# Kernel optimization log

Hardware: AMD Instinct MI355X
Metric: run time of the kernel (lower is better)

The kernel has to match this reference:

```python
import jax, jax.numpy as jnp
import numpy as np

D_MODEL = 2048
N_HEADS = 16
N_KV_HEADS = 4
HEAD_DIM = D_MODEL // N_HEADS  # 128
WINDOW = 512
THETA = 10000.0


def rotate_half(x):
    x1, x2 = jnp.split(x, 2, axis=-1)
    return jnp.concatenate((-x2, x1), axis=-1)


def rope_cos_sin(seq_len, dtype=jnp.float32):
    inv_freq = 1.0 / (THETA ** (jnp.arange(0, HEAD_DIM, 2, dtype=jnp.float32) / HEAD_DIM))
    t = jnp.arange(seq_len, dtype=jnp.float32)
    freqs = jnp.outer(t, inv_freq)              # [S, HEAD_DIM/2]
    emb = jnp.concatenate((freqs, freqs), -1)   # [S, HEAD_DIM]
    return jnp.cos(emb).astype(dtype), jnp.sin(emb).astype(dtype)


def setup_inputs() -> dict:
    key = jax.random.key(0)
    ks = jax.random.split(key, 5)
    B, S = 2, 2048
    sc = 1.0 / np.sqrt(D_MODEL)
    return {
        "x": jax.random.normal(ks[0], (B, S, D_MODEL), jnp.float32),
        "wq": jax.random.normal(ks[1], (D_MODEL, N_HEADS * HEAD_DIM), jnp.float32) * sc,
        "wk": jax.random.normal(ks[2], (D_MODEL, N_KV_HEADS * HEAD_DIM), jnp.float32) * sc,
        "wv": jax.random.normal(ks[3], (D_MODEL, N_KV_HEADS * HEAD_DIM), jnp.float32) * sc,
        "wo": jax.random.normal(ks[4], (N_HEADS * HEAD_DIM, D_MODEL), jnp.float32) * sc,
    }


def reference(x, wq, wk, wv, wo):
    B, S, _ = x.shape
    n_rep = N_HEADS // N_KV_HEADS

    q = (x @ wq).reshape(B, S, N_HEADS, HEAD_DIM).transpose(0, 2, 1, 3)      # [B,H,S,D]
    k = (x @ wk).reshape(B, S, N_KV_HEADS, HEAD_DIM).transpose(0, 2, 1, 3)   # [B,KVH,S,D]
    v = (x @ wv).reshape(B, S, N_KV_HEADS, HEAD_DIM).transpose(0, 2, 1, 3)

    cos, sin = rope_cos_sin(S, x.dtype)  # [S, D]
    q = q * cos + rotate_half(q) * sin
    k = k * cos + rotate_half(k) * sin

    # GQA: repeat kv heads to match query heads
    k = jnp.repeat(k, n_rep, axis=1)  # [B,H,S,D]
    v = jnp.repeat(v, n_rep, axis=1)

    scale = 1.0 / np.sqrt(HEAD_DIM)
    scores = jnp.einsum("bhqd,bhkd->bhqk", q, k) * scale

    # causal + sliding-window mask: allow i-WINDOW+1 <= j <= i
    i = jnp.arange(S)[:, None]
    j = jnp.arange(S)[None, :]
    allowed = (j <= i) & (j >= i - WINDOW + 1)
    scores = jnp.where(allowed, scores, -jnp.inf)

    attn = jax.nn.softmax(scores.astype(jnp.float32), axis=-1).astype(x.dtype)
    out = jnp.einsum("bhqk,bhkd->bhqd", attn, v)          # [B,H,S,D]
    out = out.transpose(0, 2, 1, 3).reshape(B, S, N_HEADS * HEAD_DIM)
    return out @ wo
```

## Files before the change

kernel.cpp:

```cpp
#include <hip/hip_runtime.h>
#include <math.h>


typedef unsigned short u16;
typedef __attribute__((ext_vector_type(4))) float f32x4;
typedef __attribute__((ext_vector_type(8))) __bf16 bf16x8;
typedef __attribute__((ext_vector_type(4))) __bf16 bf16x4;
typedef __attribute__((ext_vector_type(4))) short s16x4;
typedef __attribute__((ext_vector_type(8))) unsigned short u16x8;
typedef __attribute__((ext_vector_type(4))) unsigned short u16x4;

#define DEV static __device__ __forceinline__
#define WAITV(n) asm volatile("s_waitcnt vmcnt(" #n ")" ::: "memory")

DEV float bf2f(u16 h) {
    union { unsigned int i; float f; } x;
    x.i = ((unsigned int)h) << 16;
    return x.f;
}
DEV u16 f2bf(float f) {
    union { float f; unsigned int i; } x;
    x.f = f;
    unsigned int u = x.i;
    return (u16)((u + 0x7FFFu + ((u >> 16) & 1u)) >> 16);
}

DEV f32x4 mfma32(bf16x8 a, bf16x8 b, f32x4 c) {
    return __builtin_amdgcn_mfma_f32_16x16x32_bf16(a, b, c, 0, 0, 0);
}
DEV f32x4 mfma16(bf16x4 a, bf16x4 b, f32x4 c) {
#if __has_builtin(__builtin_amdgcn_mfma_f32_16x16x16_bf16)
    return __builtin_amdgcn_mfma_f32_16x16x16_bf16(a, b, c, 0, 0, 0);
#else
    union { bf16x4 v; s16x4 s; } ua, ub;
    ua.v = a; ub.v = b;
    return __builtin_amdgcn_mfma_f32_16x16x16bf16_1k(ua.s, ub.s, c, 0, 0, 0);
#endif
}

DEV void gload_lds16(const void* g, void* lds) {
    __builtin_amdgcn_global_load_lds(
        (const __attribute__((address_space(1))) unsigned int*)g,
        (__attribute__((address_space(3))) unsigned int*)lds, 16, 0, 0);
}

__global__ __launch_bounds__(256) void sincos_kernel(float* ct, float* st) {
    int idx = blockIdx.x * 256 + threadIdx.x;
    int s = idx >> 6, d = idx & 63;
    float inv = exp2f(-(float)d * (13.287712379549449f / 64.f));
    float a = (float)s * inv;
    float sv, cv;
    sincosf(a, &sv, &cv);
    ct[idx] = cv;
    st[idx] = sv;
}

__global__ __launch_bounds__(256) void f32_to_bf16_kernel(const float* in, u16* out, int n4) {
    int i = blockIdx.x * 256 + threadIdx.x;
    if (i >= n4) return;
    float4 v = ((const float4*)in)[i];
    u16x4 o;
    o[0] = f2bf(v.x); o[1] = f2bf(v.y); o[2] = f2bf(v.z); o[3] = f2bf(v.w);
    ((u16x4*)out)[i] = o;
}

__global__ __launch_bounds__(256) void convT4_kernel(const float* i0, const float* i1,
                                                     const float* i2, const float* i3,
                                                     u16* o0, u16* o1, u16* o2, u16* o3) {
    __shared__ float tile[32][33];
    int z = blockIdx.z;
    const float* in = (z == 0) ? i0 : (z == 1) ? i1 : (z == 2) ? i2 : i3;
    u16* out = (z == 0) ? o0 : (z == 1) ? o1 : (z == 2) ? o2 : o3;
    int ldi = (z == 1 || z == 2) ? 512 : 2048;
    if ((int)blockIdx.x >= (ldi >> 5)) return;
    int cc = threadIdx.x & 31, rb = threadIdx.x >> 5;
    long r0 = (long)blockIdx.y * 32, c0 = (long)blockIdx.x * 32;
#pragma unroll
    for (int i = 0; i < 4; i++)
        tile[rb + i * 8][cc] = in[(r0 + rb + i * 8) * (long)ldi + c0 + cc];
    __syncthreads();
#pragma unroll
    for (int i = 0; i < 4; i++)
        out[(c0 + rb + i * 8) * 2048L + r0 + cc] = f2bf(tile[cc][rb + i * 8]);
}

__global__ __launch_bounds__(256) void rope2_kernel(u16* QKV, const float* ct, const float* st) {
    int idx = blockIdx.x * 256 + threadIdx.x;
    int m, hoff, d0;
    if (idx < 524288) {
        m = idx >> 7;
        int rest = idx & 127;
        hoff = (rest >> 3) * 128;
        d0 = (rest & 7) * 8;
    } else {
        int i2 = idx - 524288;
        m = i2 >> 5;
        int rest = i2 & 31;
        hoff = 2048 + (rest >> 3) * 128;
        d0 = (rest & 7) * 8;
    }
    int s = m & 2047;
    u16* p1 = QKV + (long)m * 3072 + hoff + d0;
    u16* p2 = p1 + 64;
    u16x8 v1 = *(const u16x8*)p1;
    u16x8 v2 = *(const u16x8*)p2;
    const float* cp = ct + s * 64 + d0;
    const float* sp = st + s * 64 + d0;
    u16x8 o1, o2;
#pragma unroll
    for (int j = 0; j < 8; j++) {
        float x1 = bf2f(v1[j]), x2 = bf2f(v2[j]);
        float cc = cp[j], ss = sp[j];
        o1[j] = f2bf(x1 * cc - x2 * ss);
        o2[j] = f2bf(x2 * cc + x1 * ss);
    }
    *(u16x8*)p1 = o1;
    *(u16x8*)p2 = o2;
}

template <int BN, int WN, int EPI>
__global__ __launch_bounds__(512, 2) void gemm_pipe_kernel(const u16* __restrict__ A,
                                                           const u16* __restrict__ Bt,
                                                           void* __restrict__ Cout,
                                                           u16* __restrict__ Vt) {
    constexpr int WM = 8 / WN;
    constexpr int M_REP = (256 / WM) / 16;
    constexpr int N_REP = (BN / WN) / 16;
    constexpr int SC_B = (BN * 64) / 8192;
    constexpr int SC = 2 + SC_B;
    constexpr int BUFSZ = 8192 + BN * 32;
    constexpr int NK = 64;

    __shared__ u16 lds[4 * BUFSZ];
    const int tid = threadIdx.x;
    const int w = tid >> 6, l = tid & 63, g = l >> 4, c = l & 15;
    const int wr = w / WN, wc = w % WN;
    const long m0 = (long)blockIdx.y * 256, n0 = (long)blockIdx.x * BN;

    const u16* srcA[2];
    const u16* srcB[SC_B];
#pragma unroll
    for (int j = 0; j < 2; j++) {
        int x = j * 8192 + tid * 16;
        int row = ((x >> 10) << 4) | ((x >> 4) & 15);
        int g8 = ((x >> 8) & 3) * 8;
        srcA[j] = A + (size_t)(m0 + row) * 2048 + g8;
    }
#pragma unroll
    for (int j = 0; j < SC_B; j++) {
        int x = j * 8192 + tid * 16;
        int row = ((x >> 10) << 4) | ((x >> 4) & 15);
        int g8 = ((x >> 8) & 3) * 8;
        srcB[j] = Bt + (size_t)(n0 + row) * 2048 + g8;
    }

    auto stage = [&](int t) {
        const int bb = t & 3;
#pragma unroll
        for (int j = 0; j < 2; j++)
            gload_lds16(srcA[j] + t * 32, (void*)&lds[bb * BUFSZ + j * 4096 + tid * 8]);
#pragma unroll
        for (int j = 0; j < SC_B; j++)
            gload_lds16(srcB[j] + t * 32, (void*)&lds[bb * BUFSZ + 8192 + j * 4096 + tid * 8]);
    };

    f32x4 acc[M_REP][N_REP];
    const f32x4 zero = {0.f, 0.f, 0.f, 0.f};
#pragma unroll
    for (int i = 0; i < M_REP; i++)
#pragma unroll
        for (int j = 0; j < N_REP; j++) acc[i][j] = zero;

    stage(0);
    stage(1);
    stage(2);

    for (int kt = 0; kt < NK; ++kt) {
        const int buf = kt & 3;
        if (kt <= NK - 3) {
            if constexpr (SC == 4) WAITV(8); else WAITV(6);
        } else if (kt == NK - 2) {
            if constexpr (SC == 4) WAITV(4); else WAITV(3);
        } else {
            WAITV(0);
        }
        __builtin_amdgcn_s_barrier();
        __builtin_amdgcn_sched_barrier(0);
        asm volatile("" ::: "memory");

        if (kt + 3 < NK) stage(kt + 3);

        const u16* bp = &lds[buf * BUFSZ];
        bf16x8 af[M_REP], bfr[N_REP];
#pragma unroll
        for (int nj = 0; nj < N_REP; nj++)
            bfr[nj] = *(const bf16x8*)&bp[8192 + (wc * N_REP + nj) * 512 + l * 8];
#pragma unroll
        for (int mi = 0; mi < M_REP; mi++)
            af[mi] = *(const bf16x8*)&bp[(wr * M_REP + mi) * 512 + l * 8];

        __builtin_amdgcn_s_setprio(1);
#pragma unroll
        for (int mi = 0; mi < M_REP; mi++)
#pragma unroll
            for (int nj = 0; nj < N_REP; nj++)
                acc[mi][nj] = mfma32(af[mi], bfr[nj], acc[mi][nj]);
        __builtin_amdgcn_s_setprio(0);
    }

    if (EPI == 0) {
        float* C = (float*)Cout;
#pragma unroll
        for (int mi = 0; mi < M_REP; mi++)
#pragma unroll
            for (int nj = 0; nj < N_REP; nj++) {
                long row0 = m0 + wr * (256 / WM) + mi * 16 + g * 4;
                long col = n0 + wc * (BN / WN) + nj * 16 + c;
#pragma unroll
                for (int r = 0; r < 4; r++)
                    C[(row0 + r) * 2048 + col] = acc[mi][nj][r];
            }
    } else {
        u16* Cq = (u16*)Cout;
        if (n0 < 2560) {
#pragma unroll
            for (int mi = 0; mi < M_REP; mi++)
#pragma unroll
                for (int nj = 0; nj < N_REP; nj++) {
                    long row0 = m0 + wr * (256 / WM) + mi * 16 + g * 4;
                    long col = n0 + wc * (BN / WN) + nj * 16 + c;
#pragma unroll
                    for (int r = 0; r < 4; r++)
                        Cq[(row0 + r) * 3072 + col] = f2bf(acc[mi][nj][r]);
                }
        } else {
#pragma unroll
            for (int mi = 0; mi < M_REP; mi++)
#pragma unroll
                for (int nj = 0; nj < N_REP; nj++) {
                    long row0 = m0 + wr * (256 / WM) + mi * 16 + g * 4;
                    long b = row0 >> 11, s0 = row0 & 2047;
                    long dglob = n0 + wc * (BN / WN) + nj * 16 + c - 2560;
                    u16x4 pk;
                    pk[0] = f2bf(acc[mi][nj][0]); pk[1] = f2bf(acc[mi][nj][1]);
                    pk[2] = f2bf(acc[mi][nj][2]); pk[3] = f2bf(acc[mi][nj][3]);
                    *(u16x4*)&Vt[(b * 512 + dglob) * 2048 + s0] = pk;
                }
        }
    }
}

#define ATT_SCALE 0.08838834764831845f
#define L2E 1.4426950408889634f

__global__ __launch_bounds__(256) void attn_kernel(const u16* QKV, const u16* Vt, u16* AO) {
    __shared__ u16 Ks[64 * 128];
    __shared__ u16 Vs[128 * 64];
    const int tid = threadIdx.x;
    const int w = tid >> 6, l = tid & 63, g = l >> 4, c = l & 15;
    const int Tq = blockIdx.x;
    const int h = blockIdx.y;
    const int b = blockIdx.z;
    const int kvh = h >> 2;
    const int q0 = Tq * 64;
    const int qb = q0 + w * 16;

    bf16x8 bq[4];
    {
        const u16* qrow = QKV + (long)(b * 2048 + qb + c) * 3072 + h * 128;
#pragma unroll
        for (int kc = 0; kc < 4; kc++) bq[kc] = *(const bf16x8*)(qrow + kc * 32 + g * 8);
    }

    f32x4 acc_o[8];
    const f32x4 zero = {0.f, 0.f, 0.f, 0.f};
#pragma unroll
    for (int i = 0; i < 8; i++) acc_o[i] = zero;
    float m_run = -3.0e38f, l_run = 0.f;

    const int t_lo = (q0 > 511) ? ((q0 - 511) >> 6) : 0;
    const int t_hi = Tq;

    for (int t = t_lo; t <= t_hi; ++t) {
        const int kv0 = t * 64;
#pragma unroll
        for (int i = 0; i < 4; i++) {
            int o = (i * 256 + tid) * 16;
            int key = o >> 8;
            int cl = ((o >> 4) & 15) ^ (key & 15);
            gload_lds16(QKV + (long)(b * 2048 + kv0 + key) * 3072 + 2048 + kvh * 128 + cl * 8,
                        (void*)&Ks[(i * 256 + w * 64) * 8]);
        }
#pragma unroll
        for (int i = 0; i < 4; i++) {
            int o = (i * 256 + tid) * 16;
            int d = o >> 7;
            int cl = ((o >> 4) & 7) ^ (d & 7);
            gload_lds16(Vt + (long)((b * 4 + kvh) * 128 + d) * 2048 + kv0 + cl * 8,
                        (void*)&Vs[(i * 256 + w * 64) * 8]);
        }
        __syncthreads();

        f32x4 sacc[4];
#pragma unroll
        for (int n = 0; n < 4; n++) {
            sacc[n] = zero;
#pragma unroll
            for (int kc = 0; kc < 4; kc++) {
                int row = n * 16 + c;
                int ch = (kc * 4 + g) ^ c;
                bf16x8 kf = *(const bf16x8*)&Ks[row * 128 + ch * 8];
                sacc[n] = mfma32(kf, bq[kc], sacc[n]);
            }
        }

        const bool edge = (kv0 + 63 > qb) || (kv0 < qb + 15 - 511);
        float p[4][4];
        float m_tile = -3.0e38f;
#pragma unroll
        for (int n = 0; n < 4; n++)
#pragma unroll
            for (int r = 0; r < 4; r++) {
                float s = sacc[n][r] * ATT_SCALE;
                if (edge) {
                    int j = kv0 + n * 16 + 4 * g + r;
                    int q = qb + c;
                    if (j > q || j < q - 511) s = -__builtin_inff();
                }
                p[n][r] = s;
                m_tile = fmaxf(m_tile, s);
            }
        m_tile = fmaxf(m_tile, __shfl_xor(m_tile, 16));
        m_tile = fmaxf(m_tile, __shfl_xor(m_tile, 32));
        float m_new = fmaxf(m_run, m_tile);
        float alpha = exp2f((m_run - m_new) * L2E);
        float lsum = 0.f;
#pragma unroll
        for (int n = 0; n < 4; n++)
#pragma unroll
            for (int r = 0; r < 4; r++) {
                float e = exp2f((p[n][r] - m_new) * L2E);
                p[n][r] = e;
                lsum += e;
            }
        lsum += __shfl_xor(lsum, 16);
        lsum += __shfl_xor(lsum, 32);
        l_run = l_run * alpha + lsum;
        m_run = m_new;

        float alpha_r[4];
#pragma unroll
        for (int r = 0; r < 4; r++) alpha_r[r] = __shfl(alpha, (g << 4) + 4 * g + r);
#pragma unroll
        for (int dn = 0; dn < 8; dn++) {
            f32x4 t2 = acc_o[dn];
            t2[0] *= alpha_r[0]; t2[1] *= alpha_r[1];
            t2[2] *= alpha_r[2]; t2[3] *= alpha_r[3];
            acc_o[dn] = t2;
        }

        bf16x4 ap[4];
#pragma unroll
        for (int n = 0; n < 4; n++) {
            union { u16x4 u; bf16x4 b; } pk;
            pk.u[0] = f2bf(p[n][0]); pk.u[1] = f2bf(p[n][1]);
            pk.u[2] = f2bf(p[n][2]); pk.u[3] = f2bf(p[n][3]);
            ap[n] = pk.b;
        }

#pragma unroll
        for (int n = 0; n < 4; n++)
#pragma unroll
            for (int dn = 0; dn < 8; dn++) {
                int row = dn * 16 + c;
                int ch = (2 * n + (g >> 1)) ^ (c & 7);
                bf16x4 vf = *(const bf16x4*)&Vs[row * 64 + ch * 8 + (g & 1) * 4];
                acc_o[dn] = mfma16(ap[n], vf, acc_o[dn]);
            }
        __syncthreads();
    }

    float lr[4];
#pragma unroll
    for (int r = 0; r < 4; r++) {
        float lq = __shfl(l_run, (g << 4) + 4 * g + r);
        lr[r] = 1.f / lq;
    }
#pragma unroll
    for (int dn = 0; dn < 8; dn++)
#pragma unroll
        for (int r = 0; r < 4; r++) {
            long row = (long)(b * 2048 + qb + 4 * g + r);
            AO[row * 2048 + h * 128 + dn * 16 + c] = f2bf(acc_o[dn][r] * lr[r]);
        }
}

extern "C" void kernel_launch(void* const* d_in, const int* in_sizes, int n_in,
                              void* d_out, int out_size, void* d_ws, size_t ws_size,
                              hipStream_t stream) {
    const float* x = (const float*)d_in[0];
    const float* wq = (const float*)d_in[1];
    const float* wk = (const float*)d_in[2];
    const float* wv = (const float*)d_in[3];
    const float* wo = (const float*)d_in[4];
    float* out = (float*)d_out;

    char* ws = (char*)d_ws;
    u16* xb = (u16*)(ws);
    u16* wAll = (u16*)(ws + 16777216);
    u16* woT = (u16*)(ws + 29360128);
    u16* QKV = (u16*)(ws + 37748736);
    u16* Vt = (u16*)(ws + 62914560);
    u16* AO = (u16*)(ws + 67108864);
    float* ct = (float*)(ws + 83886080);
    float* st = (float*)(ws + 84410368);

    sincos_kernel<<<512, 256, 0, stream>>>(ct, st);
    f32_to_bf16_kernel<<<8192, 256, 0, stream>>>(x, xb, 2097152);
    convT4_kernel<<<dim3(64, 64, 4), 256, 0, stream>>>(
        wq, wk, wv, wo, wAll, wAll + (long)2048 * 2048, wAll + (long)2560 * 2048, woT);

    gemm_pipe_kernel<256, 4, 1><<<dim3(12, 16), 512, 0, stream>>>(xb, wAll, QKV, Vt);

    rope2_kernel<<<2560, 256, 0, stream>>>(QKV, ct, st);

    attn_kernel<<<dim3(32, 16, 2), 256, 0, stream>>>(QKV, Vt, AO);

    gemm_pipe_kernel<128, 2, 0><<<dim3(16, 16), 512, 0, stream>>>(AO, woT, out, nullptr);
}
```

Baseline: 208.9 us.

## Restructure GEMM into 8-wave ping-pong schedule with K=64 double buffering

Replaces the 4-stage K=32 GEMM pipeline with a double-buffered K=64 tile loop. Each iteration is split into four quadrant phases, and LDS fragment reads, half-tile global prefetches and MFMA bursts are interleaved between barriers. The aim is to overlap global-to-LDS loads and LDS reads with MFMA work and to halve the number of outer iterations. The cost is more barriers per iteration and tighter hand-coded waitcnt logic, which carries correctness and stall risk.

```diff
diff --git a/kernel.cpp b/kernel.cpp
--- a/kernel.cpp
+++ b/kernel.cpp
@@ -12,6 +12,10 @@
 
 #define DEV static __device__ __forceinline__
 #define WAITV(n) asm volatile("s_waitcnt vmcnt(" #n ")" ::: "memory")
+#define BAR __builtin_amdgcn_s_barrier()
+#define LGKM0 do { asm volatile("s_waitcnt lgkmcnt(0)" ::: "memory"); \
+                   __builtin_amdgcn_sched_barrier(0); } while (0)
+#define LGKM8 asm volatile("s_waitcnt lgkmcnt(8)" ::: "memory")
 
 DEV float bf2f(u16 h) {
     union { unsigned int i; float f; } x;
@@ -119,101 +123,158 @@
 }
 
 template <int BN, int WN, int EPI>
-__global__ __launch_bounds__(512, 2) void gemm_pipe_kernel(const u16* __restrict__ A,
-                                                           const u16* __restrict__ Bt,
-                                                           void* __restrict__ Cout,
-                                                           u16* __restrict__ Vt) {
+__global__ __launch_bounds__(512, 2) void gemm8_kernel(const u16* __restrict__ A,
+                                                       const u16* __restrict__ Bt,
+                                                       void* __restrict__ Cout,
+                                                       u16* __restrict__ Vt) {
     constexpr int WM = 8 / WN;
-    constexpr int M_REP = (256 / WM) / 16;
-    constexpr int N_REP = (BN / WN) / 16;
-    constexpr int SC_B = (BN * 64) / 8192;
-    constexpr int SC = 2 + SC_B;
-    constexpr int BUFSZ = 8192 + BN * 32;
-    constexpr int NK = 64;
-
-    __shared__ u16 lds[4 * BUFSZ];
+    constexpr int MR = 16 / WM;
+    constexpr int NR = BN / WN / 16;
+    constexpr int MH = MR / 2, NH = NR / 2;
+    constexpr int BSZ = BN * 64;
+    constexpr int BUFSZ = 16384 + BSZ;
+    constexpr int NK = 32;
+
+    __shared__ u16 lds[2 * BUFSZ];
     const int tid = threadIdx.x;
     const int w = tid >> 6, l = tid & 63, g = l >> 4, c = l & 15;
     const int wr = w / WN, wc = w % WN;
     const long m0 = (long)blockIdx.y * 256, n0 = (long)blockIdx.x * BN;
 
-    const u16* srcA[2];
-    const u16* srcB[SC_B];
-#pragma unroll
-    for (int j = 0; j < 2; j++) {
-        int x = j * 8192 + tid * 16;
-        int row = ((x >> 10) << 4) | ((x >> 4) & 15);
-        int g8 = ((x >> 8) & 3) * 8;
-        srcA[j] = A + (size_t)(m0 + row) * 2048 + g8;
-    }
-#pragma unroll
-    for (int j = 0; j < SC_B; j++) {
-        int x = j * 8192 + tid * 16;
-        int row = ((x >> 10) << 4) | ((x >> 4) & 15);
-        int g8 = ((x >> 8) & 3) * 8;
-        srcB[j] = Bt + (size_t)(n0 + row) * 2048 + g8;
-    }
-
-    auto stage = [&](int t) {
-        const int bb = t & 3;
-#pragma unroll
-        for (int j = 0; j < 2; j++)
-            gload_lds16(srcA[j] + t * 32, (void*)&lds[bb * BUFSZ + j * 4096 + tid * 8]);
-#pragma unroll
-        for (int j = 0; j < SC_B; j++)
-            gload_lds16(srcB[j] + t * 32, (void*)&lds[bb * BUFSZ + 8192 + j * 4096 + tid * 8]);
+    const int rowS = ((tid >> 6) << 4) | (tid & 15);
+    const int ggS = ((tid >> 4) & 3) * 8;
+
+    auto stageA = [&](int t, int h, int j) {
+        gload_lds16(A + (size_t)(m0 + h * 128 + rowS) * 2048 + t * 64 + j * 32 + ggS,
+                    (void*)&lds[(t & 1) * BUFSZ + h * 8192 + j * 4096 + (tid << 3)]);
     };
-
-    f32x4 acc[M_REP][N_REP];
+    auto stageB = [&](int t, int h, int j) {
+        if constexpr (BN == 256) {
+            gload_lds16(Bt + (size_t)(n0 + h * 128 + rowS) * 2048 + t * 64 + j * 32 + ggS,
+                        (void*)&lds[(t & 1) * BUFSZ + 16384 + h * 8192 + j * 4096 + (tid << 3)]);
+        } else {
+            gload_lds16(Bt + (size_t)(n0 + h * 64 + (((tid >> 6) & 3) << 4) + (tid & 15)) * 2048
+                            + t * 64 + (tid >> 8) * 32 + ggS,
+                        (void*)&lds[(t & 1) * BUFSZ + 16384 + h * 4096 + (tid << 3)]);
+        }
+    };
+    auto stageAh = [&](int t, int h) { stageA(t, h, 0); stageA(t, h, 1); };
+    auto stageBh = [&](int t, int h) {
+        if constexpr (BN == 256) { stageB(t, h, 0); stageB(t, h, 1); }
+        else stageB(t, h, 0);
+    };
+
+    auto readA = [&](int b, int mi, int kk) -> bf16x8 {
+        int rg = wr * MR + mi;
+        return *(const bf16x8*)&lds[b * BUFSZ + (rg >> 3) * 8192 + kk * 4096 +
+                                    (rg & 7) * 512 + l * 8];
+    };
+    auto readB = [&](int b, int nj, int kk) -> bf16x8 {
+        int rg = wc * NR + nj;
+        if constexpr (BN == 256)
+            return *(const bf16x8*)&lds[b * BUFSZ + 16384 + (rg >> 3) * 8192 + kk * 4096 +
+                                        (rg & 7) * 512 + l * 8];
+        else
+            return *(const bf16x8*)&lds[b * BUFSZ + 16384 + (rg >> 2) * 4096 + kk * 2048 +
+                                        (rg & 3) * 512 + l * 8];
+    };
+
+    f32x4 acc[MR][NR];
     const f32x4 zero = {0.f, 0.f, 0.f, 0.f};
 #pragma unroll
-    for (int i = 0; i < M_REP; i++)
-#pragma unroll
-        for (int j = 0; j < N_REP; j++) acc[i][j] = zero;
-
-    stage(0);
-    stage(1);
-    stage(2);
-
-    for (int kt = 0; kt < NK; ++kt) {
-        const int buf = kt & 3;
-        if (kt <= NK - 3) {
-            if constexpr (SC == 4) WAITV(8); else WAITV(6);
-        } else if (kt == NK - 2) {
-            if constexpr (SC == 4) WAITV(4); else WAITV(3);
-        } else {
-            WAITV(0);
-        }
-        __builtin_amdgcn_s_barrier();
-        __builtin_amdgcn_sched_barrier(0);
-        asm volatile("" ::: "memory");
-
-        if (kt + 3 < NK) stage(kt + 3);
-
-        const u16* bp = &lds[buf * BUFSZ];
-        bf16x8 af[M_REP], bfr[N_REP];
-#pragma unroll
-        for (int nj = 0; nj < N_REP; nj++)
-            bfr[nj] = *(const bf16x8*)&bp[8192 + (wc * N_REP + nj) * 512 + l * 8];
-#pragma unroll
-        for (int mi = 0; mi < M_REP; mi++)
-            af[mi] = *(const bf16x8*)&bp[(wr * M_REP + mi) * 512 + l * 8];
-
+    for (int i = 0; i < MR; i++)
+#pragma unroll
+        for (int j = 0; j < NR; j++) acc[i][j] = zero;
+
+    stageAh(0, 0); stageAh(0, 1);
+    stageBh(0, 0); stageBh(0, 1);
+    stageAh(1, 0);
+    WAITV(2);
+    BAR;
+
+    bf16x8 fa[MH][2], fb[NH][2];
+
+    for (int t = 0; t < NK; ++t) {
+        const int b = t & 1;
+#pragma unroll
+        for (int mi = 0; mi < MH; mi++)
+#pragma unroll
+            for (int kk = 0; kk < 2; kk++) fa[mi][kk] = readA(b, mi, kk);
+#pragma unroll
+        for (int nj = 0; nj < NH; nj++)
+#pragma unroll
+            for (int kk = 0; kk < 2; kk++) fb[nj][kk] = readB(b, nj, kk);
+        if (t + 1 < NK) stageAh(t + 1, 1);
+        if constexpr (2 * (MH + NH) >= 12) LGKM8;
+        BAR; LGKM0;
         __builtin_amdgcn_s_setprio(1);
 #pragma unroll
-        for (int mi = 0; mi < M_REP; mi++)
-#pragma unroll
-            for (int nj = 0; nj < N_REP; nj++)
-                acc[mi][nj] = mfma32(af[mi], bfr[nj], acc[mi][nj]);
+        for (int mi = 0; mi < MH; mi++)
+#pragma unroll
+            for (int nj = 0; nj < NH; nj++)
+#pragma unroll
+                for (int kk = 0; kk < 2; kk++)
+                    acc[mi][nj] = mfma32(fa[mi][kk], fb[nj][kk], acc[mi][nj]);
         __builtin_amdgcn_s_setprio(0);
+        BAR;
+#pragma unroll
+        for (int nj = 0; nj < NH; nj++)
+#pragma unroll
+            for (int kk = 0; kk < 2; kk++) fb[nj][kk] = readB(b, NH + nj, kk);
+        if (t + 1 < NK) stageBh(t + 1, 0);
+        BAR; LGKM0;
+        __builtin_amdgcn_s_setprio(1);
+#pragma unroll
+        for (int mi = 0; mi < MH; mi++)
+#pragma unroll
+            for (int nj = 0; nj < NH; nj++)
+#pragma unroll
+                for (int kk = 0; kk < 2; kk++)
+                    acc[mi][NH + nj] = mfma32(fa[mi][kk], fb[nj][kk], acc[mi][NH + nj]);
+        __builtin_amdgcn_s_setprio(0);
+        BAR;
+#pragma unroll
+        for (int mi = 0; mi < MH; mi++)
+#pragma unroll
+            for (int kk = 0; kk < 2; kk++) fa[mi][kk] = readA(b, MH + mi, kk);
+        if (t + 1 < NK) stageBh(t + 1, 1);
+        BAR; LGKM0;
+        __builtin_amdgcn_s_setprio(1);
+#pragma unroll
+        for (int mi = 0; mi < MH; mi++)
+#pragma unroll
+            for (int nj = 0; nj < NH; nj++)
+#pragma unroll
+                for (int kk = 0; kk < 2; kk++)
+                    acc[MH + mi][NH + nj] = mfma32(fa[mi][kk], fb[nj][kk], acc[MH + mi][NH + nj]);
+        __builtin_amdgcn_s_setprio(0);
+        BAR;
+#pragma unroll
+        for (int nj = 0; nj < NH; nj++)
+#pragma unroll
+            for (int kk = 0; kk < 2; kk++) fb[nj][kk] = readB(b, nj, kk);
+        if (t + 2 < NK) stageAh(t + 2, 0);
+        BAR; LGKM0;
+        __builtin_amdgcn_s_setprio(1);
+#pragma unroll
+        for (int mi = 0; mi < MH; mi++)
+#pragma unroll
+            for (int nj = 0; nj < NH; nj++)
+#pragma unroll
+                for (int kk = 0; kk < 2; kk++)
+                    acc[MH + mi][nj] = mfma32(fa[mi][kk], fb[nj][kk], acc[MH + mi][nj]);
+        __builtin_amdgcn_s_setprio(0);
+        if (t <= NK - 3) { WAITV(2); }
+        else if (t == NK - 2) { WAITV(0); }
+        BAR;
     }
 
     if (EPI == 0) {
         float* C = (float*)Cout;
 #pragma unroll
-        for (int mi = 0; mi < M_REP; mi++)
-#pragma unroll
-            for (int nj = 0; nj < N_REP; nj++) {
+        for (int mi = 0; mi < MR; mi++)
+#pragma unroll
+            for (int nj = 0; nj < NR; nj++) {
                 long row0 = m0 + wr * (256 / WM) + mi * 16 + g * 4;
                 long col = n0 + wc * (BN / WN) + nj * 16 + c;
 #pragma unroll
@@ -224,9 +285,9 @@
         u16* Cq = (u16*)Cout;
         if (n0 < 2560) {
 #pragma unroll
-            for (int mi = 0; mi < M_REP; mi++)
-#pragma unroll
-                for (int nj = 0; nj < N_REP; nj++) {
+            for (int mi = 0; mi < MR; mi++)
+#pragma unroll
+                for (int nj = 0; nj < NR; nj++) {
                     long row0 = m0 + wr * (256 / WM) + mi * 16 + g * 4;
                     long col = n0 + wc * (BN / WN) + nj * 16 + c;
 #pragma unroll
@@ -235,9 +296,9 @@
                 }
         } else {
 #pragma unroll
-            for (int mi = 0; mi < M_REP; mi++)
-#pragma unroll
-                for (int nj = 0; nj < N_REP; nj++) {
+            for (int mi = 0; mi < MR; mi++)
+#pragma unroll
+                for (int nj = 0; nj < NR; nj++) {
                     long row0 = m0 + wr * (256 / WM) + mi * 16 + g * 4;
                     long b = row0 >> 11, s0 = row0 & 2047;
                     long dglob = n0 + wc * (BN / WN) + nj * 16 + c - 2560;
@@ -420,11 +481,11 @@
     convT4_kernel<<<dim3(64, 64, 4), 256, 0, stream>>>(
         wq, wk, wv, wo, wAll, wAll + (long)2048 * 2048, wAll + (long)2560 * 2048, woT);
 
-    gemm_pipe_kernel<256, 4, 1><<<dim3(12, 16), 512, 0, stream>>>(xb, wAll, QKV, Vt);
+    gemm8_kernel<256, 4, 1><<<dim3(12, 16), 512, 0, stream>>>(xb, wAll, QKV, Vt);
 
     rope2_kernel<<<2560, 256, 0, stream>>>(QKV, ct, st);
 
     attn_kernel<<<dim3(32, 16, 2), 256, 0, stream>>>(QKV, Vt, AO);
 
-    gemm_pipe_kernel<128, 2, 0><<<dim3(16, 16), 512, 0, stream>>>(AO, woT, out, nullptr);
-}
+    gemm8_kernel<128, 2, 0><<<dim3(16, 16), 512, 0, stream>>>(AO, woT, out, nullptr);
+}
```

Result: no change. 208.1 us (-0.4%).
